# Optimization experiments

Measured on AMD Instinct MI355X. Metric: run time of the kernel, lower is better.

Reference implementation:

```python
import jax, jax.numpy as jnp
import numpy as np

TOP_K = 2  # config.n_expert_per_token


def setup_inputs() -> dict:
    key = jax.random.key(0)
    ks = jax.random.split(key, 5)
    B, T, C, E, F = 2, 2048, 2048, 8, 1024
    scale = 0.02
    return {
        "x": jax.random.normal(ks[0], (B, T, C), jnp.float32),
        "w_router": jax.random.normal(ks[1], (C, E), jnp.float32) * scale,
        "w1": jax.random.normal(ks[2], (E, C, F), jnp.float32) * scale,  # fc_1 (gate proj)
        "w3": jax.random.normal(ks[3], (E, C, F), jnp.float32) * scale,  # fc_2 (up proj)
        "w2": jax.random.normal(ks[4], (E, F, C), jnp.float32) * scale,  # proj (down)
    }


def reference(x, w_router, w1, w3, w2):
    B, T, C = x.shape
    xt = x.reshape(-1, C)                                  # [N, C]
    N = xt.shape[0]
    E = w_router.shape[1]
    # Router: topk logits, softmax over the selected k in fp32
    logits = xt @ w_router                                 # [N, E]
    top_vals, top_idx = jax.lax.top_k(logits, TOP_K)       # [N, k]
    probs = jax.nn.softmax(top_vals.astype(jnp.float32), axis=1).astype(xt.dtype)
    # Per-token per-expert combine weight (0 for unselected experts).
    # topk indices are distinct per token, so scatter-add == scatter-set.
    w = jnp.zeros((N, E), xt.dtype).at[jnp.arange(N)[:, None], top_idx].add(probs)  # [N, E]
    # Dense grouped SwiGLU expert MLPs; zero-weight tokens contribute nothing.
    g = jnp.einsum('nc,ecf->enf', xt, w1)                  # [E, N, F]
    u = jnp.einsum('nc,ecf->enf', xt, w3)                  # [E, N, F]
    h = jax.nn.silu(g) * u                                 # [E, N, F]
    outs = jnp.einsum('enf,efc->enc', h, w2)               # [E, N, C]
    y = jnp.einsum('enc,ne->nc', outs, w)                  # weighted combine
    return y.reshape(B, T, C)
```

## Files before the change

kernel.cpp:

```cpp
#include <hip/hip_runtime.h>
#include <hip/hip_bf16.h>
#include <stdint.h>

#define N_TOK 4096
#define CDIM 2048
#define EXP 8
#define FDIM 1024

typedef __attribute__((ext_vector_type(4))) float f32x4;
typedef __attribute__((ext_vector_type(8))) short bf16x8;

__device__ __forceinline__ void gl2lds16(const short* g, short* l) {
  __builtin_amdgcn_global_load_lds(
      (const __attribute__((address_space(1))) void*)g,
      (__attribute__((address_space(3))) void*)l, 16, 0, 0);
}

__global__ __launch_bounds__(256) void transpose_to_bf16(
    const float* __restrict__ in, __hip_bfloat16* __restrict__ out, int R, int Cc) {
  __shared__ float tile[64][65];
  int e = blockIdx.z;
  const float* ip = in + (size_t)e * R * Cc;
  __hip_bfloat16* op = out + (size_t)e * R * Cc;
  int r0 = blockIdx.y * 64, c0 = blockIdx.x * 64;
  int t = threadIdx.x;
  {
    int r = t >> 2, cb = (t & 3) * 16;
    const float* src = ip + (size_t)(r0 + r) * Cc + c0 + cb;
#pragma unroll
    for (int i = 0; i < 4; i++) {
      float4 v = *(const float4*)(src + i * 4);
      tile[cb + i * 4 + 0][r] = v.x;
      tile[cb + i * 4 + 1][r] = v.y;
      tile[cb + i * 4 + 2][r] = v.z;
      tile[cb + i * 4 + 3][r] = v.w;
    }
  }
  __syncthreads();
  {
    int c = t >> 2, sb = (t & 3) * 16;
    union { int4 v[2]; __hip_bfloat16 h[16]; } u;
#pragma unroll
    for (int j = 0; j < 16; j++) u.h[j] = __float2bfloat16(tile[c][sb + j]);
    __hip_bfloat16* dst = op + (size_t)(c0 + c) * R + r0 + sb;
    *(int4*)(dst) = u.v[0];
    *(int4*)(dst + 8) = u.v[1];
  }
}

__global__ __launch_bounds__(256) void router_kernel(
    const float* __restrict__ x, const float* __restrict__ wr,
    __hip_bfloat16* __restrict__ x_bf, int* __restrict__ counts,
    int* __restrict__ pair_expert, float* __restrict__ pair_prob) {
  int tok = blockIdx.x;
  const float* xr = x + (size_t)tok * CDIM;
  int t = threadIdx.x;
  float acc[EXP];
#pragma unroll
  for (int e = 0; e < EXP; e++) acc[e] = 0.f;
#pragma unroll
  for (int j = 0; j < 8; j++) {
    int c = j * 256 + t;
    float xv = xr[c];
    x_bf[(size_t)tok * CDIM + c] = __float2bfloat16(xv);
    const float4* wr4 = (const float4*)(wr + (size_t)c * EXP);
    float4 wa = wr4[0], wb = wr4[1];
    acc[0] += xv * wa.x; acc[1] += xv * wa.y; acc[2] += xv * wa.z; acc[3] += xv * wa.w;
    acc[4] += xv * wb.x; acc[5] += xv * wb.y; acc[6] += xv * wb.z; acc[7] += xv * wb.w;
  }
#pragma unroll
  for (int e = 0; e < EXP; e++) {
#pragma unroll
    for (int off = 32; off > 0; off >>= 1) acc[e] += __shfl_down(acc[e], off, 64);
  }
  __shared__ float wsum[4][EXP];
  int wid = t >> 6, lane = t & 63;
  if (lane == 0) {
#pragma unroll
    for (int e = 0; e < EXP; e++) wsum[wid][e] = acc[e];
  }
  __syncthreads();
  if (t == 0) {
    float lg[EXP];
#pragma unroll
    for (int e = 0; e < EXP; e++) lg[e] = wsum[0][e] + wsum[1][e] + wsum[2][e] + wsum[3][e];
    int i0 = 0;
#pragma unroll
    for (int e = 1; e < EXP; e++) if (lg[e] > lg[i0]) i0 = e;
    int i1 = (i0 == 0) ? 1 : 0;
#pragma unroll
    for (int e = 0; e < EXP; e++) if (e != i0 && lg[e] > lg[i1]) i1 = e;
    float e1 = __expf(lg[i1] - lg[i0]);
    float p0 = 1.f / (1.f + e1);
    pair_expert[tok * 2 + 0] = i0;
    pair_expert[tok * 2 + 1] = i1;
    pair_prob[tok * 2 + 0] = p0;
    pair_prob[tok * 2 + 1] = e1 * p0;
    atomicAdd(&counts[i0], 1);
    atomicAdd(&counts[i1], 1);
  }
}

__global__ void scan_kernel(const int* __restrict__ counts, int* __restrict__ bases) {
  if (threadIdx.x == 0) {
    int s = 0;
    for (int e = 0; e < EXP; e++) { bases[e] = s; s += counts[e]; }
  }
}

__global__ __launch_bounds__(256) void scatter_kernel(
    const int* __restrict__ pair_expert, const int* __restrict__ bases,
    int* __restrict__ cursors, int* __restrict__ lists, int* __restrict__ slot_map) {
  int tok = blockIdx.x * 256 + threadIdx.x;
  if (tok >= N_TOK) return;
#pragma unroll
  for (int k = 0; k < 2; k++) {
    int e = pair_expert[tok * 2 + k];
    int pos = atomicAdd(&cursors[e], 1);
    int slot = bases[e] + pos;
    lists[slot] = tok * 2 + k;
    slot_map[tok * 2 + k] = slot;
  }
}

__global__ __launch_bounds__(256) void gemm1_kernel(
    const __hip_bfloat16* __restrict__ xbf, const __hip_bfloat16* __restrict__ w1t,
    const __hip_bfloat16* __restrict__ w3t, const int* __restrict__ counts,
    const int* __restrict__ bases, const int* __restrict__ lists,
    __hip_bfloat16* __restrict__ h) {
  int e = blockIdx.z;
  int n_e = counts[e];
  int m0 = blockIdx.y * 128;
  if (m0 >= n_e) return;
  int base = bases[e];
  int f0 = blockIdx.x * 64;

  __shared__ short As[128 * 32];
  __shared__ short B1s[64 * 32];
  __shared__ short B3s[64 * 32];

  int t = threadIdx.x;
  int lane = t & 63, wid = t >> 6;

  int rowA = t >> 2, sub = (t & 3) * 8;
  int r1 = m0 + rowA, r2 = m0 + 64 + rowA;
  int tok1 = lists[base + ((r1 < n_e) ? r1 : 0)] >> 1;
  int tok2 = lists[base + ((r2 < n_e) ? r2 : 0)] >> 1;

  const short* xs = (const short*)xbf;
  const short* ag1 = xs + (size_t)tok1 * CDIM + sub;
  const short* ag2 = xs + (size_t)tok2 * CDIM + sub;
  const short* b1g = (const short*)w1t + (size_t)e * FDIM * CDIM + (size_t)(f0 + rowA) * CDIM + sub;
  const short* b3g = (const short*)w3t + (size_t)e * FDIM * CDIM + (size_t)(f0 + rowA) * CDIM + sub;

  short* al1 = As + wid * 512;
  short* al2 = As + 2048 + wid * 512;
  short* b1l = B1s + wid * 512;
  short* b3l = B3s + wid * 512;

  f32x4 zero = {0.f, 0.f, 0.f, 0.f};
  f32x4 accg[4][2], accu[4][2];
#pragma unroll
  for (int i = 0; i < 4; i++)
#pragma unroll
    for (int j = 0; j < 2; j++) { accg[i][j] = zero; accu[i][j] = zero; }

  int wm = (wid & 1) * 64, wf = (wid >> 1) * 32;
  int kq = (lane >> 4) * 8;
  int rsel = lane & 15;

  for (int kk = 0; kk < CDIM; kk += 32) {
    __syncthreads();
    gl2lds16(ag1 + kk, al1);
    gl2lds16(ag2 + kk, al2);
    gl2lds16(b1g + kk, b1l);
    gl2lds16(b3g + kk, b3l);
    __syncthreads();
    bf16x8 af[4], b1f[2], b3f[2];
#pragma unroll
    for (int i = 0; i < 4; i++)
      af[i] = *(const bf16x8*)(As + (wm + i * 16 + rsel) * 32 + kq);
#pragma unroll
    for (int j = 0; j < 2; j++) {
      b1f[j] = *(const bf16x8*)(B1s + (wf + j * 16 + rsel) * 32 + kq);
      b3f[j] = *(const bf16x8*)(B3s + (wf + j * 16 + rsel) * 32 + kq);
    }
#pragma unroll
    for (int i = 0; i < 4; i++)
#pragma unroll
      for (int j = 0; j < 2; j++) {
        accg[i][j] = __builtin_amdgcn_mfma_f32_16x16x32_bf16(af[i], b1f[j], accg[i][j], 0, 0, 0);
        accu[i][j] = __builtin_amdgcn_mfma_f32_16x16x32_bf16(af[i], b3f[j], accu[i][j], 0, 0, 0);
      }
  }

  int col = lane & 15;
  int rbase = (lane >> 4) * 4;
#pragma unroll
  for (int i = 0; i < 4; i++) {
#pragma unroll
    for (int r = 0; r < 4; r++) {
      int m = m0 + wm + i * 16 + rbase + r;
      if (m < n_e) {
        size_t hrow = (size_t)(base + m) * FDIM;
#pragma unroll
        for (int j = 0; j < 2; j++) {
          int f = f0 + wf + j * 16 + col;
          float g = accg[i][j][r];
          float u = accu[i][j][r];
          float sg = g / (1.f + __expf(-g));
          h[hrow + f] = __float2bfloat16(sg * u);
        }
      }
    }
  }
}

__global__ __launch_bounds__(256) void gemm2_kernel(
    const __hip_bfloat16* __restrict__ h, const __hip_bfloat16* __restrict__ w2t,
    const int* __restrict__ counts, const int* __restrict__ bases,
    float* __restrict__ o_pair) {
  int e = blockIdx.z;
  int n_e = counts[e];
  int m0 = blockIdx.y * 128;
  if (m0 >= n_e) return;
  int base = bases[e];
  int c0 = blockIdx.x * 128;

  __shared__ short As[128 * 32];
  __shared__ short Bs[128 * 32];

  int t = threadIdx.x;
  int lane = t & 63, wid = t >> 6;

  int rowA = t >> 2, sub = (t & 3) * 8;
  int hr1 = base + m0 + rowA;
  int hr2 = base + m0 + 64 + rowA;
  if (hr1 > 2 * N_TOK - 1) hr1 = 2 * N_TOK - 1;
  if (hr2 > 2 * N_TOK - 1) hr2 = 2 * N_TOK - 1;
  const short* hp = (const short*)h;
  const short* bp = (const short*)w2t + (size_t)e * CDIM * FDIM;
  const short* ag1 = hp + (size_t)hr1 * FDIM + sub;
  const short* ag2 = hp + (size_t)hr2 * FDIM + sub;
  const short* bg1 = bp + (size_t)(c0 + rowA) * FDIM + sub;
  const short* bg2 = bp + (size_t)(c0 + 64 + rowA) * FDIM + sub;

  short* al1 = As + wid * 512;
  short* al2 = As + 2048 + wid * 512;
  short* bl1 = Bs + wid * 512;
  short* bl2 = Bs + 2048 + wid * 512;

  f32x4 zero = {0.f, 0.f, 0.f, 0.f};
  f32x4 acc[4][4];
#pragma unroll
  for (int i = 0; i < 4; i++)
#pragma unroll
    for (int j = 0; j < 4; j++) acc[i][j] = zero;

  int wm = (wid & 1) * 64, wn = (wid >> 1) * 64;
  int kq = (lane >> 4) * 8;
  int rsel = lane & 15;

  for (int kk = 0; kk < FDIM; kk += 32) {
    __syncthreads();
    gl2lds16(ag1 + kk, al1);
    gl2lds16(ag2 + kk, al2);
    gl2lds16(bg1 + kk, bl1);
    gl2lds16(bg2 + kk, bl2);
    __syncthreads();
    bf16x8 af[4], bfr[4];
#pragma unroll
    for (int i = 0; i < 4; i++)
      af[i] = *(const bf16x8*)(As + (wm + i * 16 + rsel) * 32 + kq);
#pragma unroll
    for (int j = 0; j < 4; j++)
      bfr[j] = *(const bf16x8*)(Bs + (wn + j * 16 + rsel) * 32 + kq);
#pragma unroll
    for (int i = 0; i < 4; i++)
#pragma unroll
      for (int j = 0; j < 4; j++)
        acc[i][j] = __builtin_amdgcn_mfma_f32_16x16x32_bf16(af[i], bfr[j], acc[i][j], 0, 0, 0);
  }

  int col = lane & 15;
  int rbase = (lane >> 4) * 4;
#pragma unroll
  for (int i = 0; i < 4; i++) {
#pragma unroll
    for (int r = 0; r < 4; r++) {
      int m = m0 + wm + i * 16 + rbase + r;
      if (m < n_e) {
        size_t orow = (size_t)(base + m) * CDIM;
#pragma unroll
        for (int j = 0; j < 4; j++) {
          int c = c0 + wn + j * 16 + col;
          o_pair[orow + c] = acc[i][j][r];
        }
      }
    }
  }
}

__global__ __launch_bounds__(256) void combine_kernel(
    const float* __restrict__ o_pair, const int* __restrict__ slot_map,
    const float* __restrict__ pair_prob, float* __restrict__ out) {
  int tok = blockIdx.x;
  int s0 = slot_map[tok * 2 + 0], s1 = slot_map[tok * 2 + 1];
  float p0 = pair_prob[tok * 2 + 0], p1 = pair_prob[tok * 2 + 1];
  const float4* r0 = (const float4*)(o_pair + (size_t)s0 * CDIM);
  const float4* r1 = (const float4*)(o_pair + (size_t)s1 * CDIM);
  float4* op = (float4*)(out + (size_t)tok * CDIM);
  int t = threadIdx.x;
#pragma unroll
  for (int j = 0; j < 2; j++) {
    int i = j * 256 + t;
    float4 a = r0[i], b = r1[i];
    float4 c;
    c.x = p0 * a.x + p1 * b.x;
    c.y = p0 * a.y + p1 * b.y;
    c.z = p0 * a.z + p1 * b.z;
    c.w = p0 * a.w + p1 * b.w;
    op[i] = c;
  }
}

extern "C" void kernel_launch(void* const* d_in, const int* in_sizes, int n_in,
                              void* d_out, int out_size, void* d_ws, size_t ws_size,
                              hipStream_t stream) {
  const float* x  = (const float*)d_in[0];
  const float* wr = (const float*)d_in[1];
  const float* w1 = (const float*)d_in[2];
  const float* w3 = (const float*)d_in[3];
  const float* w2 = (const float*)d_in[4];
  float* out = (float*)d_out;

  char* ws = (char*)d_ws;
  __hip_bfloat16* x_bf = (__hip_bfloat16*)(ws);
  __hip_bfloat16* h    = (__hip_bfloat16*)(ws + 16777216);
  __hip_bfloat16* w1t  = (__hip_bfloat16*)(ws + 33554432);
  __hip_bfloat16* w3t  = (__hip_bfloat16*)(ws + 67108864);
  __hip_bfloat16* w2t  = (__hip_bfloat16*)(ws + 100663296);
  float* o_pair = (float*)(ws + 33554432);
  int* counts  = (int*)(ws + 134217728);
  int* bases   = counts + 8;
  int* cursors = counts + 16;
  int* pair_expert = (int*)(ws + 134217728 + 128);
  float* pair_prob = (float*)(ws + 134217728 + 128 + 32768);
  int* lists       = (int*)(ws + 134217728 + 128 + 65536);
  int* slot_map    = (int*)(ws + 134217728 + 128 + 98304);

  hipMemsetAsync(counts, 0, 128, stream);

  transpose_to_bf16<<<dim3(FDIM / 64, CDIM / 64, EXP), 256, 0, stream>>>(w1, w1t, CDIM, FDIM);
  transpose_to_bf16<<<dim3(FDIM / 64, CDIM / 64, EXP), 256, 0, stream>>>(w3, w3t, CDIM, FDIM);
  transpose_to_bf16<<<dim3(CDIM / 64, FDIM / 64, EXP), 256, 0, stream>>>(w2, w2t, FDIM, CDIM);

  router_kernel<<<N_TOK, 256, 0, stream>>>(x, wr, x_bf, counts, pair_expert, pair_prob);
  scan_kernel<<<1, 64, 0, stream>>>(counts, bases);
  scatter_kernel<<<N_TOK / 256, 256, 0, stream>>>(pair_expert, bases, cursors, lists, slot_map);

  gemm1_kernel<<<dim3(FDIM / 64, N_TOK / 128, EXP), 256, 0, stream>>>(
      x_bf, w1t, w3t, counts, bases, lists, h);
  gemm2_kernel<<<dim3(CDIM / 128, N_TOK / 128, EXP), 256, 0, stream>>>(
      h, w2t, counts, bases, o_pair);
  combine_kernel<<<N_TOK, 256, 0, stream>>>(o_pair, slot_map, pair_prob, out);
}
```

Measured before the change: 618.5 us.

## Double-buffer LDS tiles and XOR-swizzle layout in both expert GEMMs

Both grouped GEMM kernels now keep two LDS buffers and prefetch the next K-tile with global_load_lds while MFMAs run on the current one. An explicit vmcnt wait and raw s_barrier replace the pair of __syncthreads per iteration. The 16-byte chunk index within each row is also XOR-swizzled on load and read to cut LDS bank conflicts. This doubles shared memory per block, which may lower occupancy, and relies on hand-placed waitcnt and barrier ordering being correct.

```diff
diff --git a/kernel.cpp b/kernel.cpp
--- a/kernel.cpp
+++ b/kernel.cpp
@@ -15,6 +15,9 @@
       (const __attribute__((address_space(1))) void*)g,
       (__attribute__((address_space(3))) void*)l, 16, 0, 0);
 }
+
+#define SBAR() __builtin_amdgcn_s_barrier()
+#define SCHED0() __builtin_amdgcn_sched_barrier(0)
 
 __global__ __launch_bounds__(256) void transpose_to_bf16(
     const float* __restrict__ in, __hip_bfloat16* __restrict__ out, int R, int Cc) {
@@ -135,14 +138,16 @@
   int base = bases[e];
   int f0 = blockIdx.x * 64;
 
-  __shared__ short As[128 * 32];
-  __shared__ short B1s[64 * 32];
-  __shared__ short B3s[64 * 32];
+  __shared__ short As[2 * 4096];
+  __shared__ short B1s[2 * 2048];
+  __shared__ short B3s[2 * 2048];
 
   int t = threadIdx.x;
   int lane = t & 63, wid = t >> 6;
 
-  int rowA = t >> 2, sub = (t & 3) * 8;
+  int rowA = t >> 2;
+  int cswz = (t & 3) ^ ((rowA >> 1) & 3);
+  int sub = cswz * 8;
   int r1 = m0 + rowA, r2 = m0 + 64 + rowA;
   int tok1 = lists[base + ((r1 < n_e) ? r1 : 0)] >> 1;
   int tok2 = lists[base + ((r2 < n_e) ? r2 : 0)] >> 1;
@@ -153,10 +158,12 @@
   const short* b1g = (const short*)w1t + (size_t)e * FDIM * CDIM + (size_t)(f0 + rowA) * CDIM + sub;
   const short* b3g = (const short*)w3t + (size_t)e * FDIM * CDIM + (size_t)(f0 + rowA) * CDIM + sub;
 
-  short* al1 = As + wid * 512;
-  short* al2 = As + 2048 + wid * 512;
-  short* b1l = B1s + wid * 512;
-  short* b3l = B3s + wid * 512;
+  int aoff = wid * 512;
+
+  gl2lds16(ag1, As + aoff);
+  gl2lds16(ag2, As + 2048 + aoff);
+  gl2lds16(b1g, B1s + aoff);
+  gl2lds16(b3g, B3s + aoff);
 
   f32x4 zero = {0.f, 0.f, 0.f, 0.f};
   f32x4 accg[4][2], accu[4][2];
@@ -166,24 +173,34 @@
     for (int j = 0; j < 2; j++) { accg[i][j] = zero; accu[i][j] = zero; }
 
   int wm = (wid & 1) * 64, wf = (wid >> 1) * 32;
-  int kq = (lane >> 4) * 8;
   int rsel = lane & 15;
-
-  for (int kk = 0; kk < CDIM; kk += 32) {
-    __syncthreads();
-    gl2lds16(ag1 + kk, al1);
-    gl2lds16(ag2 + kk, al2);
-    gl2lds16(b1g + kk, b1l);
-    gl2lds16(b3g + kk, b3l);
-    __syncthreads();
+  int kq_swz = (((lane >> 4) ^ ((lane >> 1) & 3))) * 8;
+
+#pragma unroll 2
+  for (int tt = 0; tt < CDIM / 32; ++tt) {
+    int cb = tt & 1;
+    if (tt < CDIM / 32 - 1) {
+      int nb = cb ^ 1;
+      int kk = (tt + 1) * 32;
+      gl2lds16(ag1 + kk, As + nb * 4096 + aoff);
+      gl2lds16(ag2 + kk, As + nb * 4096 + 2048 + aoff);
+      gl2lds16(b1g + kk, B1s + nb * 2048 + aoff);
+      gl2lds16(b3g + kk, B3s + nb * 2048 + aoff);
+      asm volatile("s_waitcnt vmcnt(4)" ::: "memory");
+    } else {
+      asm volatile("s_waitcnt vmcnt(0)" ::: "memory");
+    }
+    SCHED0();
+    SBAR();
+    SCHED0();
     bf16x8 af[4], b1f[2], b3f[2];
 #pragma unroll
     for (int i = 0; i < 4; i++)
-      af[i] = *(const bf16x8*)(As + (wm + i * 16 + rsel) * 32 + kq);
+      af[i] = *(const bf16x8*)(As + cb * 4096 + (wm + i * 16 + rsel) * 32 + kq_swz);
 #pragma unroll
     for (int j = 0; j < 2; j++) {
-      b1f[j] = *(const bf16x8*)(B1s + (wf + j * 16 + rsel) * 32 + kq);
-      b3f[j] = *(const bf16x8*)(B3s + (wf + j * 16 + rsel) * 32 + kq);
+      b1f[j] = *(const bf16x8*)(B1s + cb * 2048 + (wf + j * 16 + rsel) * 32 + kq_swz);
+      b3f[j] = *(const bf16x8*)(B3s + cb * 2048 + (wf + j * 16 + rsel) * 32 + kq_swz);
     }
 #pragma unroll
     for (int i = 0; i < 4; i++)
@@ -192,6 +209,8 @@
         accg[i][j] = __builtin_amdgcn_mfma_f32_16x16x32_bf16(af[i], b1f[j], accg[i][j], 0, 0, 0);
         accu[i][j] = __builtin_amdgcn_mfma_f32_16x16x32_bf16(af[i], b3f[j], accu[i][j], 0, 0, 0);
       }
+    SCHED0();
+    SBAR();
   }
 
   int col = lane & 15;
@@ -227,13 +246,15 @@
   int base = bases[e];
   int c0 = blockIdx.x * 128;
 
-  __shared__ short As[128 * 32];
-  __shared__ short Bs[128 * 32];
+  __shared__ short As[2 * 4096];
+  __shared__ short Bs[2 * 4096];
 
   int t = threadIdx.x;
   int lane = t & 63, wid = t >> 6;
 
-  int rowA = t >> 2, sub = (t & 3) * 8;
+  int rowA = t >> 2;
+  int cswz = (t & 3) ^ ((rowA >> 1) & 3);
+  int sub = cswz * 8;
   int hr1 = base + m0 + rowA;
   int hr2 = base + m0 + 64 + rowA;
   if (hr1 > 2 * N_TOK - 1) hr1 = 2 * N_TOK - 1;
@@ -245,10 +266,12 @@
   const short* bg1 = bp + (size_t)(c0 + rowA) * FDIM + sub;
   const short* bg2 = bp + (size_t)(c0 + 64 + rowA) * FDIM + sub;
 
-  short* al1 = As + wid * 512;
-  short* al2 = As + 2048 + wid * 512;
-  short* bl1 = Bs + wid * 512;
-  short* bl2 = Bs + 2048 + wid * 512;
+  int aoff = wid * 512;
+
+  gl2lds16(ag1, As + aoff);
+  gl2lds16(ag2, As + 2048 + aoff);
+  gl2lds16(bg1, Bs + aoff);
+  gl2lds16(bg2, Bs + 2048 + aoff);
 
   f32x4 zero = {0.f, 0.f, 0.f, 0.f};
   f32x4 acc[4][4];
@@ -258,28 +281,40 @@
     for (int j = 0; j < 4; j++) acc[i][j] = zero;
 
   int wm = (wid & 1) * 64, wn = (wid >> 1) * 64;
-  int kq = (lane >> 4) * 8;
   int rsel = lane & 15;
-
-  for (int kk = 0; kk < FDIM; kk += 32) {
-    __syncthreads();
-    gl2lds16(ag1 + kk, al1);
-    gl2lds16(ag2 + kk, al2);
-    gl2lds16(bg1 + kk, bl1);
-    gl2lds16(bg2 + kk, bl2);
-    __syncthreads();
+  int kq_swz = (((lane >> 4) ^ ((lane >> 1) & 3))) * 8;
+
+#pragma unroll 2
+  for (int tt = 0; tt < FDIM / 32; ++tt) {
+    int cb = tt & 1;
+    if (tt < FDIM / 32 - 1) {
+      int nb = cb ^ 1;
+      int kk = (tt + 1) * 32;
+      gl2lds16(ag1 + kk, As + nb * 4096 + aoff);
+      gl2lds16(ag2 + kk, As + nb * 4096 + 2048 + aoff);
+      gl2lds16(bg1 + kk, Bs + nb * 4096 + aoff);
+      gl2lds16(bg2 + kk, Bs + nb * 4096 + 2048 + aoff);
+      asm volatile("s_waitcnt vmcnt(4)" ::: "memory");
+    } else {
+      asm volatile("s_waitcnt vmcnt(0)" ::: "memory");
+    }
+    SCHED0();
+    SBAR();
+    SCHED0();
     bf16x8 af[4], bfr[4];
 #pragma unroll
     for (int i = 0; i < 4; i++)
-      af[i] = *(const bf16x8*)(As + (wm + i * 16 + rsel) * 32 + kq);
+      af[i] = *(const bf16x8*)(As + cb * 4096 + (wm + i * 16 + rsel) * 32 + kq_swz);
 #pragma unroll
     for (int j = 0; j < 4; j++)
-      bfr[j] = *(const bf16x8*)(Bs + (wn + j * 16 + rsel) * 32 + kq);
+      bfr[j] = *(const bf16x8*)(Bs + cb * 4096 + (wn + j * 16 + rsel) * 32 + kq_swz);
 #pragma unroll
     for (int i = 0; i < 4; i++)
 #pragma unroll
       for (int j = 0; j < 4; j++)
         acc[i][j] = __builtin_amdgcn_mfma_f32_16x16x32_bf16(af[i], bfr[j], acc[i][j], 0, 0, 0);
+    SCHED0();
+    SBAR();
   }
 
   int col = lane & 15;
```

After: 614.2 us. No clear change (-0.7%).

## Compact expert tile list for grouped GEMMs and swizzle LDS to avoid bank conflicts

Applied to the files above, without the earlier changes.

The scan kernel now builds a compact list of (expert, row-offset) tiles, and both grouped GEMMs launch over this list. Previously the grid covered every expert times the maximum number of row tiles, and most blocks exited early. LDS columns are also XOR-swizzled per row, on both the global-to-LDS writes and the fragment reads, to cut bank conflicts. MAX_TILES=72 is a fixed upper bound on the tile count and assumes the sum of ceil(count/128) stays at or below 72.

```diff
diff --git a/kernel.cpp b/kernel.cpp
--- a/kernel.cpp
+++ b/kernel.cpp
@@ -6,6 +6,7 @@
 #define CDIM 2048
 #define EXP 8
 #define FDIM 1024
+#define MAX_TILES 72
 
 typedef __attribute__((ext_vector_type(4))) float f32x4;
 typedef __attribute__((ext_vector_type(8))) short bf16x8;
@@ -101,10 +102,16 @@
   }
 }
 
-__global__ void scan_kernel(const int* __restrict__ counts, int* __restrict__ bases) {
+__global__ void scan_kernel(const int* __restrict__ counts, int* __restrict__ bases,
+                            int* __restrict__ tiles, int* __restrict__ ntiles) {
   if (threadIdx.x == 0) {
     int s = 0;
     for (int e = 0; e < EXP; e++) { bases[e] = s; s += counts[e]; }
+    int nt = 0;
+    for (int e = 0; e < EXP; e++)
+      for (int m0 = 0; m0 < counts[e]; m0 += 128)
+        tiles[nt++] = (e << 20) | m0;
+    ntiles[0] = nt;
   }
 }
 
@@ -127,22 +134,27 @@
     const __hip_bfloat16* __restrict__ xbf, const __hip_bfloat16* __restrict__ w1t,
     const __hip_bfloat16* __restrict__ w3t, const int* __restrict__ counts,
     const int* __restrict__ bases, const int* __restrict__ lists,
+    const int* __restrict__ tiles, const int* __restrict__ ntiles,
     __hip_bfloat16* __restrict__ h) {
-  int e = blockIdx.z;
+  int y = blockIdx.y;
+  if (y >= ntiles[0]) return;
+  int packed = tiles[y];
+  int e = packed >> 20;
+  int m0 = packed & 0xFFFFF;
   int n_e = counts[e];
-  int m0 = blockIdx.y * 128;
-  if (m0 >= n_e) return;
   int base = bases[e];
   int f0 = blockIdx.x * 64;
 
-  __shared__ short As[128 * 32];
-  __shared__ short B1s[64 * 32];
-  __shared__ short B3s[64 * 32];
+  __shared__ short As[4096];
+  __shared__ short B1s[2048];
+  __shared__ short B3s[2048];
 
   int t = threadIdx.x;
   int lane = t & 63, wid = t >> 6;
 
-  int rowA = t >> 2, sub = (t & 3) * 8;
+  int rowA = t >> 2;
+  int cswz = (t & 3) ^ ((rowA >> 1) & 3);
+  int sub = cswz * 8;
   int r1 = m0 + rowA, r2 = m0 + 64 + rowA;
   int tok1 = lists[base + ((r1 < n_e) ? r1 : 0)] >> 1;
   int tok2 = lists[base + ((r2 < n_e) ? r2 : 0)] >> 1;
@@ -153,10 +165,7 @@
   const short* b1g = (const short*)w1t + (size_t)e * FDIM * CDIM + (size_t)(f0 + rowA) * CDIM + sub;
   const short* b3g = (const short*)w3t + (size_t)e * FDIM * CDIM + (size_t)(f0 + rowA) * CDIM + sub;
 
-  short* al1 = As + wid * 512;
-  short* al2 = As + 2048 + wid * 512;
-  short* b1l = B1s + wid * 512;
-  short* b3l = B3s + wid * 512;
+  int aoff = wid * 512;
 
   f32x4 zero = {0.f, 0.f, 0.f, 0.f};
   f32x4 accg[4][2], accu[4][2];
@@ -166,24 +175,24 @@
     for (int j = 0; j < 2; j++) { accg[i][j] = zero; accu[i][j] = zero; }
 
   int wm = (wid & 1) * 64, wf = (wid >> 1) * 32;
-  int kq = (lane >> 4) * 8;
   int rsel = lane & 15;
+  int kq_swz = (((lane >> 4) ^ ((lane >> 1) & 3))) * 8;
 
   for (int kk = 0; kk < CDIM; kk += 32) {
     __syncthreads();
-    gl2lds16(ag1 + kk, al1);
-    gl2lds16(ag2 + kk, al2);
-    gl2lds16(b1g + kk, b1l);
-    gl2lds16(b3g + kk, b3l);
+    gl2lds16(ag1 + kk, As + aoff);
+    gl2lds16(ag2 + kk, As + 2048 + aoff);
+    gl2lds16(b1g + kk, B1s + aoff);
+    gl2lds16(b3g + kk, B3s + aoff);
     __syncthreads();
     bf16x8 af[4], b1f[2], b3f[2];
 #pragma unroll
     for (int i = 0; i < 4; i++)
-      af[i] = *(const bf16x8*)(As + (wm + i * 16 + rsel) * 32 + kq);
+      af[i] = *(const bf16x8*)(As + (wm + i * 16 + rsel) * 32 + kq_swz);
 #pragma unroll
     for (int j = 0; j < 2; j++) {
-      b1f[j] = *(const bf16x8*)(B1s + (wf + j * 16 + rsel) * 32 + kq);
-      b3f[j] = *(const bf16x8*)(B3s + (wf + j * 16 + rsel) * 32 + kq);
+      b1f[j] = *(const bf16x8*)(B1s + (wf + j * 16 + rsel) * 32 + kq_swz);
+      b3f[j] = *(const bf16x8*)(B3s + (wf + j * 16 + rsel) * 32 + kq_swz);
     }
 #pragma unroll
     for (int i = 0; i < 4; i++)
@@ -219,21 +228,26 @@
 __global__ __launch_bounds__(256) void gemm2_kernel(
     const __hip_bfloat16* __restrict__ h, const __hip_bfloat16* __restrict__ w2t,
     const int* __restrict__ counts, const int* __restrict__ bases,
+    const int* __restrict__ tiles, const int* __restrict__ ntiles,
     float* __restrict__ o_pair) {
-  int e = blockIdx.z;
+  int y = blockIdx.y;
+  if (y >= ntiles[0]) return;
+  int packed = tiles[y];
+  int e = packed >> 20;
+  int m0 = packed & 0xFFFFF;
   int n_e = counts[e];
-  int m0 = blockIdx.y * 128;
-  if (m0 >= n_e) return;
   int base = bases[e];
   int c0 = blockIdx.x * 128;
 
-  __shared__ short As[128 * 32];
-  __shared__ short Bs[128 * 32];
+  __shared__ short As[4096];
+  __shared__ short Bs[4096];
 
   int t = threadIdx.x;
   int lane = t & 63, wid = t >> 6;
 
-  int rowA = t >> 2, sub = (t & 3) * 8;
+  int rowA = t >> 2;
+  int cswz = (t & 3) ^ ((rowA >> 1) & 3);
+  int sub = cswz * 8;
   int hr1 = base + m0 + rowA;
   int hr2 = base + m0 + 64 + rowA;
   if (hr1 > 2 * N_TOK - 1) hr1 = 2 * N_TOK - 1;
@@ -245,10 +259,7 @@
   const short* bg1 = bp + (size_t)(c0 + rowA) * FDIM + sub;
   const short* bg2 = bp + (size_t)(c0 + 64 + rowA) * FDIM + sub;
 
-  short* al1 = As + wid * 512;
-  short* al2 = As + 2048 + wid * 512;
-  short* bl1 = Bs + wid * 512;
-  short* bl2 = Bs + 2048 + wid * 512;
+  int aoff = wid * 512;
 
   f32x4 zero = {0.f, 0.f, 0.f, 0.f};
   f32x4 acc[4][4];
@@ -258,23 +269,23 @@
     for (int j = 0; j < 4; j++) acc[i][j] = zero;
 
   int wm = (wid & 1) * 64, wn = (wid >> 1) * 64;
-  int kq = (lane >> 4) * 8;
   int rsel = lane & 15;
+  int kq_swz = (((lane >> 4) ^ ((lane >> 1) & 3))) * 8;
 
   for (int kk = 0; kk < FDIM; kk += 32) {
     __syncthreads();
-    gl2lds16(ag1 + kk, al1);
-    gl2lds16(ag2 + kk, al2);
-    gl2lds16(bg1 + kk, bl1);
-    gl2lds16(bg2 + kk, bl2);
+    gl2lds16(ag1 + kk, As + aoff);
+    gl2lds16(ag2 + kk, As + 2048 + aoff);
+    gl2lds16(bg1 + kk, Bs + aoff);
+    gl2lds16(bg2 + kk, Bs + 2048 + aoff);
     __syncthreads();
     bf16x8 af[4], bfr[4];
 #pragma unroll
     for (int i = 0; i < 4; i++)
-      af[i] = *(const bf16x8*)(As + (wm + i * 16 + rsel) * 32 + kq);
+      af[i] = *(const bf16x8*)(As + (wm + i * 16 + rsel) * 32 + kq_swz);
 #pragma unroll
     for (int j = 0; j < 4; j++)
-      bfr[j] = *(const bf16x8*)(Bs + (wn + j * 16 + rsel) * 32 + kq);
+      bfr[j] = *(const bf16x8*)(Bs + (wn + j * 16 + rsel) * 32 + kq_swz);
 #pragma unroll
     for (int i = 0; i < 4; i++)
 #pragma unroll
@@ -344,10 +355,12 @@
   int* counts  = (int*)(ws + 134217728);
   int* bases   = counts + 8;
   int* cursors = counts + 16;
+  int* ntiles  = counts + 24;
   int* pair_expert = (int*)(ws + 134217728 + 128);
   float* pair_prob = (float*)(ws + 134217728 + 128 + 32768);
   int* lists       = (int*)(ws + 134217728 + 128 + 65536);
   int* slot_map    = (int*)(ws + 134217728 + 128 + 98304);
+  int* tiles       = (int*)(ws + 134217728 + 128 + 131072);
 
   hipMemsetAsync(counts, 0, 128, stream);
 
@@ -356,12 +369,12 @@
   transpose_to_bf16<<<dim3(CDIM / 64, FDIM / 64, EXP), 256, 0, stream>>>(w2, w2t, FDIM, CDIM);
 
   router_kernel<<<N_TOK, 256, 0, stream>>>(x, wr, x_bf, counts, pair_expert, pair_prob);
-  scan_kernel<<<1, 64, 0, stream>>>(counts, bases);
+  scan_kernel<<<1, 64, 0, stream>>>(counts, bases, tiles, ntiles);
   scatter_kernel<<<N_TOK / 256, 256, 0, stream>>>(pair_expert, bases, cursors, lists, slot_map);
 
-  gemm1_kernel<<<dim3(FDIM / 64, N_TOK / 128, EXP), 256, 0, stream>>>(
-      x_bf, w1t, w3t, counts, bases, lists, h);
-  gemm2_kernel<<<dim3(CDIM / 128, N_TOK / 128, EXP), 256, 0, stream>>>(
-      h, w2t, counts, bases, o_pair);
+  gemm1_kernel<<<dim3(FDIM / 64, MAX_TILES), 256, 0, stream>>>(
+      x_bf, w1t, w3t, counts, bases, lists, tiles, ntiles, h);
+  gemm2_kernel<<<dim3(CDIM / 128, MAX_TILES), 256, 0, stream>>>(
+      h, w2t, counts, bases, tiles, ntiles, o_pair);
   combine_kernel<<<N_TOK, 256, 0, stream>>>(o_pair, slot_map, pair_prob, out);
 }
```

Result: no change. 613.5 us (-0.8%).
